# Kernel optimization log

Hardware: AMD Instinct MI355X
Metric: run time of the kernel (lower is better)

The kernel has to match this reference:

```python
import jax, jax.numpy as jnp
import numpy as np


def _conv1x1(x, w, b):
    # x: [B, Cin, T, H, W], w: [Cout, Cin], b: [Cout] -> [B, Cout, T, H, W]
    return jnp.einsum('bcthw,oc->bothw', x, w) + b[None, :, None, None, None]


def setup_inputs() -> dict:
    key = jax.random.key(0)
    ks = jax.random.split(key, 9)
    B, Ci, T, H, W = 2, 128, 4, 32, 32
    Co = 64
    s_in = 1.0 / np.sqrt(Ci)
    s_out = 1.0 / np.sqrt(Co)
    return {
        'z': jax.random.normal(ks[0], (B, Ci, T, H, W), dtype=jnp.float32),
        'w_theta': jax.random.uniform(ks[1], (Co, Ci), jnp.float32, -s_in, s_in),
        'b_theta': jax.random.uniform(ks[2], (Co,), jnp.float32, -s_in, s_in),
        'w_phi': jax.random.uniform(ks[3], (Co, Ci), jnp.float32, -s_in, s_in),
        'b_phi': jax.random.uniform(ks[4], (Co,), jnp.float32, -s_in, s_in),
        'w_psi': jax.random.uniform(ks[5], (Co, Ci), jnp.float32, -s_in, s_in),
        'b_psi': jax.random.uniform(ks[6], (Co,), jnp.float32, -s_in, s_in),
        'w_v': jax.random.uniform(ks[7], (Ci, Co), jnp.float32, -s_out, s_out),
        'b_v': jax.random.uniform(ks[8], (Ci,), jnp.float32, -s_out, s_out),
    }


def reference(z, w_theta, b_theta, w_phi, b_phi, w_psi, b_psi, w_v, b_v):
    B, Ci, T, H, W = z.shape
    Co = w_theta.shape[0]
    N = T * H * W
    # 1x1 conv projections, flattened to [B, Co, N]
    theta = _conv1x1(z, w_theta, b_theta).reshape(B, Co, N)
    phi = _conv1x1(z, w_phi, b_phi).reshape(B, Co, N)
    psi = _conv1x1(z, w_psi, b_psi).reshape(B, Co, N)
    # g = phi^T @ psi : [B, N, N]; normalize with ReLU(g / N)
    g = jnp.einsum('bcn,bcm->bnm', phi, psi)
    norm_g = jax.nn.relu(g / jnp.asarray(N, z.dtype))
    # tmp = norm_g @ theta^T -> [B, N, Co] -> [B, Co, T, H, W]
    tmp = jnp.einsum('bnm,bcm->bcn', norm_g, theta).reshape(B, Co, T, H, W)
    vg = _conv1x1(tmp, w_v, b_v)
    return vg + z
```

## Files before the change

### kernel.cpp

```cpp
#include <hip/hip_runtime.h>


#define NSEQ 4096
#define CI 128
#define CO 64

typedef __attribute__((ext_vector_type(8))) short bf16x8;
typedef __attribute__((ext_vector_type(4))) short bf16x4;
typedef __attribute__((ext_vector_type(4))) float f32x4;
typedef __attribute__((ext_vector_type(16))) float f32x16;

static __device__ inline short f2bf(float f) {
  union { float f; unsigned u; } v; v.f = f;
  unsigned r = v.u + 0x7fffu + ((v.u >> 16) & 1u);
  return (short)(r >> 16);
}
static __device__ inline float bf2f(short s) {
  union { unsigned u; float f; } v; v.u = ((unsigned)(unsigned short)s) << 16;
  return v.f;
}

#define MFMA1632(a, b, c) __builtin_amdgcn_mfma_f32_16x16x32_bf16(a, b, c, 0, 0, 0)
#define MFMA3216(a, b, c) __builtin_amdgcn_mfma_f32_32x32x16_bf16(a, b, c, 0, 0, 0)

#if __has_builtin(__builtin_amdgcn_mfma_f32_16x16x16bf16_1k)
static __device__ inline f32x4 mfma16(bf16x4 a, bf16x4 b, f32x4 c) {
  return __builtin_amdgcn_mfma_f32_16x16x16bf16_1k(a, b, c, 0, 0, 0);
}
#else
static __device__ inline f32x4 mfma16(bf16x4 a, bf16x4 b, f32x4 c) {
  asm("v_mfma_f32_16x16x16_bf16 %0, %1, %2, %0" : "+v"(c) : "v"(a), "v"(b));
  return c;
}
#endif

static __device__ inline unsigned cvt_pk_bf16(float lo, float hi) {
  unsigned d;
  asm("v_cvt_pk_bf16_f32 %0, %1, %2" : "=v"(d) : "v"(lo), "v"(hi));
  return d;
}
static __device__ inline void pl32swap(unsigned& a, unsigned& b) {
  asm("v_permlane32_swap_b32 %0, %1" : "+v"(a), "+v"(b));
}

__global__ __launch_bounds__(256, 2) void proj_kernel(
    const float* __restrict__ z,
    const float* __restrict__ w_th, const float* __restrict__ b_th,
    const float* __restrict__ w_ph, const float* __restrict__ b_ph,
    const float* __restrict__ w_ps, const float* __restrict__ b_ps,
    short* __restrict__ Qg, short* __restrict__ Kg, short* __restrict__ Vt)
{
  const int bid = blockIdx.x;
  const int b = bid >> 8;
  const int n0 = (bid & 255) * 16;
  const int t = threadIdx.x;
  const int w = t >> 6, l = t & 63, lr = l & 15, lg = l >> 4;
  const f32x4 zero4 = {0.f, 0.f, 0.f, 0.f};

  bf16x8 zf[4];
#pragma unroll
  for (int ks = 0; ks < 4; ++ks) {
    const float* zp = z + (size_t)(b * CI + ks * 32 + lg * 8) * NSEQ + n0 + lr;
    float tmp[8];
#pragma unroll
    for (int j = 0; j < 8; ++j) tmp[j] = zp[(size_t)j * NSEQ];
#pragma unroll
    for (int j = 0; j < 8; ++j) zf[ks][j] = f2bf(tmp[j]);
  }

  {
    const float* Wm[2] = {w_ph, w_ps};
    const float* Bm[2] = {b_ph, b_ps};
    short*       Dm[2] = {Qg, Kg};
#pragma unroll
    for (int mt = 0; mt < 2; ++mt) {
      const float sc = (mt == 0) ? (1.0f / 4096.0f) : 1.0f;
      f32x4 acc = zero4;
#pragma unroll
      for (int ks = 0; ks < 4; ++ks) {
        const float* wp = Wm[mt] + (size_t)(w * 16 + lr) * CI + ks * 32 + lg * 8;
        f32x4 x0 = *(const f32x4*)wp;
        f32x4 x1 = *(const f32x4*)(wp + 4);
        bf16x8 wf;
#pragma unroll
        for (int j = 0; j < 4; ++j) { wf[j] = f2bf(x0[j] * sc); wf[4 + j] = f2bf(x1[j] * sc); }
        acc = MFMA1632(wf, zf[ks], acc);
      }
      const f32x4 bias4 = *(const f32x4*)(Bm[mt] + w * 16 + lg * 4);
      bf16x4 pk;
#pragma unroll
      for (int r = 0; r < 4; ++r) pk[r] = f2bf(acc[r] + bias4[r] * sc);
      *(bf16x4*)(Dm[mt] + (size_t)(b * NSEQ + n0 + lr) * CO + w * 16 + lg * 4) = pk;
    }
  }

  {
    f32x4 acc = zero4;
#pragma unroll
    for (int ks = 0; ks < 4; ++ks) {
      const float* wp = w_th + (size_t)(w * 16 + lr) * CI + ks * 32 + lg * 8;
      f32x4 x0 = *(const f32x4*)wp;
      f32x4 x1 = *(const f32x4*)(wp + 4);
      bf16x8 wtf;
#pragma unroll
      for (int j = 0; j < 4; ++j) { wtf[j] = f2bf(x0[j]); wtf[4 + j] = f2bf(x1[j]); }
      acc = MFMA1632(zf[ks], wtf, acc);
    }
    const float bias = b_th[w * 16 + lr];
    bf16x4 pk;
#pragma unroll
    for (int r = 0; r < 4; ++r) pk[r] = f2bf(acc[r] + bias);
    *(bf16x4*)(Vt + (size_t)(b * CO + w * 16 + lr) * NSEQ + n0 + lg * 4) = pk;
  }
}

__global__ __launch_bounds__(256, 3) void attn_kernel(
    const short* __restrict__ Qg, const short* __restrict__ Kg,
    const short* __restrict__ Vt, short* __restrict__ Opart)
{
  __shared__ float red[2][4096];

  const int bid = blockIdx.x;
  const int ms = bid & 7;
  const int rr = bid >> 3;
  const int b  = rr & 1;
  const int nt = rr >> 1;
  const int n0 = nt * 64;
  const int t = threadIdx.x;
  const int w = t >> 6, l = t & 63, lc = l & 31, h = l >> 5;
  const int mw = ms * 512 + w * 128;

  bf16x8 qf[2][4];
  {
    const short* qb = Qg + (size_t)(b * NSEQ + n0 + lc) * CO + h * 8;
#pragma unroll
    for (int nsub = 0; nsub < 2; ++nsub)
#pragma unroll
      for (int ks = 0; ks < 4; ++ks)
        qf[nsub][ks] = *(const bf16x8*)(qb + (size_t)nsub * 32 * CO + ks * 16);
  }

  f32x16 oacc[2][2];
#pragma unroll
  for (int i = 0; i < 2; ++i)
#pragma unroll
    for (int j = 0; j < 2; ++j)
#pragma unroll
      for (int e = 0; e < 16; ++e) oacc[i][j][e] = 0.f;

#pragma unroll
  for (int it = 0; it < 4; ++it) {
    const int m0 = mw + it * 32;

    bf16x8 kf[4];
    {
      const short* kb = Kg + (size_t)(b * NSEQ + m0 + lc) * CO + h * 8;
#pragma unroll
      for (int ks = 0; ks < 4; ++ks) kf[ks] = *(const bf16x8*)(kb + ks * 16);
    }

    f32x16 s0, s1;
#pragma unroll
    for (int e = 0; e < 16; ++e) { s0[e] = 0.f; s1[e] = 0.f; }
#pragma unroll
    for (int ks = 0; ks < 4; ++ks) s0 = MFMA3216(kf[ks], qf[0][ks], s0);
    unsigned pk0[8];
#pragma unroll
    for (int q = 0; q < 8; ++q)
      pk0[q] = cvt_pk_bf16(fmaxf(s0[2 * q], 0.f), fmaxf(s0[2 * q + 1], 0.f));
#pragma unroll
    for (int ks = 0; ks < 4; ++ks) s1 = MFMA3216(kf[ks], qf[1][ks], s1);
    unsigned pk1[8];
#pragma unroll
    for (int q = 0; q < 8; ++q)
      pk1[q] = cvt_pk_bf16(fmaxf(s1[2 * q], 0.f), fmaxf(s1[2 * q + 1], 0.f));

    const short* vb = Vt + (size_t)(b * CO + lc) * NSEQ + m0 + h * 8;
#pragma unroll
    for (int kw = 0; kw < 2; ++kw) {
      unsigned x0 = pk0[4 * kw + 0], y0 = pk0[4 * kw + 2];
      unsigned x1 = pk0[4 * kw + 1], y1 = pk0[4 * kw + 3];
      pl32swap(x0, y0); pl32swap(x1, y1);
      union { unsigned u[4]; bf16x8 v; } pb0 = {{x0, x1, y0, y1}};
      unsigned u0 = pk1[4 * kw + 0], v0 = pk1[4 * kw + 2];
      unsigned u1 = pk1[4 * kw + 1], v1 = pk1[4 * kw + 3];
      pl32swap(u0, v0); pl32swap(u1, v1);
      union { unsigned u[4]; bf16x8 v; } pb1 = {{u0, u1, v0, v1}};

      bf16x8 vf0 = *(const bf16x8*)(vb + kw * 16);
      bf16x8 vf1 = *(const bf16x8*)(vb + (size_t)32 * NSEQ + kw * 16);
      oacc[0][0] = MFMA3216(vf0, pb0.v, oacc[0][0]);
      oacc[1][0] = MFMA3216(vf1, pb0.v, oacc[1][0]);
      oacc[0][1] = MFMA3216(vf0, pb1.v, oacc[0][1]);
      oacc[1][1] = MFMA3216(vf1, pb1.v, oacc[1][1]);
    }
  }

  if (!(w & 1)) {
#pragma unroll
    for (int osub = 0; osub < 2; ++osub)
#pragma unroll
      for (int nsub = 0; nsub < 2; ++nsub)
#pragma unroll
        for (int rb = 0; rb < 4; ++rb) {
          f32x4 v;
#pragma unroll
          for (int r = 0; r < 4; ++r) v[r] = oacc[osub][nsub][rb * 4 + r];
          const int o = osub * 32 + rb * 8 + h * 4;
          const int n = nsub * 32 + lc;
          const int os = o ^ ((n & 15) << 2);
          *(f32x4*)&red[w >> 1][n * 64 + os] = v;
        }
  }
  __syncthreads();
  if (w & 1) {
#pragma unroll
    for (int osub = 0; osub < 2; ++osub)
#pragma unroll
      for (int nsub = 0; nsub < 2; ++nsub)
#pragma unroll
        for (int rb = 0; rb < 4; ++rb) {
          const int o = osub * 32 + rb * 8 + h * 4;
          const int n = nsub * 32 + lc;
          const int os = o ^ ((n & 15) << 2);
          float* p = &red[w >> 1][n * 64 + os];
          f32x4 v = *(f32x4*)p;
#pragma unroll
          for (int r = 0; r < 4; ++r) v[r] += oacc[osub][nsub][rb * 4 + r];
          *(f32x4*)p = v;
        }
  }
  __syncthreads();

  short* gout = Opart + (size_t)((b * 64 + nt) * 8 + ms) * 4096;
#pragma unroll
  for (int pass = 0; pass < 4; ++pass) {
    const int lin = pass * 1024 + t * 4;
    const int n = lin >> 6, os4 = lin & 63;
    f32x4 v0 = *(f32x4*)&red[0][lin];
    f32x4 v1 = *(f32x4*)&red[1][lin];
    const int o = os4 ^ ((n & 15) << 2);
    bf16x4 pkv;
#pragma unroll
    for (int r = 0; r < 4; ++r) pkv[r] = f2bf(v0[r] + v1[r]);
    *(bf16x4*)(gout + n * 64 + o) = pkv;
  }
}

__global__ __launch_bounds__(256, 2) void epi_kernel(
    const short* __restrict__ Opart, const float* __restrict__ w_v,
    const float* __restrict__ b_v, const float* __restrict__ z,
    float* __restrict__ out)
{
  __shared__ float Olds[32 * 65];

  const int bid = blockIdx.x;
  const int b = bid >> 7;
  const int nt32 = bid & 127;
  const int nt = nt32 >> 1, nh2 = nt32 & 1;
  const int t = threadIdx.x;

  {
    const short* src = Opart + (size_t)((b * 64 + nt) * 8) * 4096 + nh2 * 32 * 64;
    const int n = t >> 3, o8 = (t & 7) * 8;
    float acc[8];
#pragma unroll
    for (int j = 0; j < 8; ++j) acc[j] = 0.f;
#pragma unroll
    for (int p = 0; p < 8; ++p) {
      bf16x8 vv = *(const bf16x8*)(src + (size_t)p * 4096 + n * 64 + o8);
#pragma unroll
      for (int j = 0; j < 8; ++j) acc[j] += bf2f(vv[j]);
    }
#pragma unroll
    for (int j = 0; j < 8; ++j) Olds[n * 65 + o8 + j] = acc[j];
  }
  __syncthreads();

  const int w = t >> 6, l = t & 63, lr = l & 15, lg = l >> 4;
  const f32x4 zero4 = {0.f, 0.f, 0.f, 0.f};

  bf16x4 of[2][4];
#pragma unroll
  for (int nh = 0; nh < 2; ++nh)
#pragma unroll
    for (int osub = 0; osub < 4; ++osub)
#pragma unroll
      for (int j = 0; j < 4; ++j)
        of[nh][osub][j] = f2bf(Olds[(nh * 16 + lr) * 65 + osub * 16 + lg * 4 + j]);

#pragma unroll
  for (int c2 = 0; c2 < 2; ++c2) {
    const int cis = w * 2 + c2;
    bf16x4 wfr[4];
#pragma unroll
    for (int osub = 0; osub < 4; ++osub) {
      f32x4 wl = *(const f32x4*)(w_v + (size_t)(cis * 16 + lr) * CO + osub * 16 + lg * 4);
#pragma unroll
      for (int j = 0; j < 4; ++j) wfr[osub][j] = f2bf(wl[j]);
    }
    const f32x4 bv4 = *(const f32x4*)(b_v + cis * 16 + lg * 4);
#pragma unroll
    for (int nh = 0; nh < 2; ++nh) {
      f32x4 e = zero4;
#pragma unroll
      for (int osub = 0; osub < 4; ++osub)
        e = mfma16(wfr[osub], of[nh][osub], e);
#pragma unroll
      for (int r = 0; r < 4; ++r) {
        const int ci = cis * 16 + lg * 4 + r;
        const size_t off = (size_t)(b * CI + ci) * NSEQ + nt32 * 32 + nh * 16 + lr;
        out[off] = e[r] + z[off] + bv4[r];
      }
    }
  }
}

extern "C" void kernel_launch(void* const* d_in, const int* in_sizes, int n_in,
                              void* d_out, int out_size, void* d_ws, size_t ws_size,
                              hipStream_t stream) {
  const float* z    = (const float*)d_in[0];
  const float* w_th = (const float*)d_in[1];
  const float* b_th = (const float*)d_in[2];
  const float* w_ph = (const float*)d_in[3];
  const float* b_ph = (const float*)d_in[4];
  const float* w_ps = (const float*)d_in[5];
  const float* b_ps = (const float*)d_in[6];
  const float* w_v  = (const float*)d_in[7];
  const float* b_v  = (const float*)d_in[8];
  float* out = (float*)d_out;

  short* Qg = (short*)d_ws;
  short* Kg = Qg + 2 * NSEQ * CO;
  short* Vt = Kg + 2 * NSEQ * CO;
  short* Opart = Vt + 2 * NSEQ * CO;

  proj_kernel<<<512, 256, 0, stream>>>(z, w_th, b_th, w_ph, b_ph, w_ps, b_ps,
                                       Qg, Kg, Vt);
  attn_kernel<<<1024, 256, 0, stream>>>(Qg, Kg, Vt, Opart);
  epi_kernel<<<256, 256, 0, stream>>>(Opart, w_v, b_v, z, out);
}
```

Before: 108.9 us.

## Halve attention query tile to 32 rows and double grid for more occupancy

The attention kernel now processes 32 query rows per block instead of 64. That halves the register accumulators and the shared reduction buffer, raises the launch-bounds occupancy hint from 3 to 4, and doubles the grid to 2048 blocks. The epilogue is re-tiled to 16 columns per block with 512 blocks to match the new partial-output layout. The aim is better latency hiding and wave fill across CUs. In exchange, every K and V fragment is now loaded from memory twice as often for the same query work, and there are twice as many partial tiles.

Result: slower. 121.3 us (+11.4%).

```diff
diff --git a/kernel.cpp b/kernel.cpp
--- a/kernel.cpp
+++ b/kernel.cpp
@@ -114,39 +114,34 @@
   }
 }
 
-__global__ __launch_bounds__(256, 3) void attn_kernel(
+__global__ __launch_bounds__(256, 4) void attn_kernel(
     const short* __restrict__ Qg, const short* __restrict__ Kg,
     const short* __restrict__ Vt, short* __restrict__ Opart)
 {
-  __shared__ float red[2][4096];
+  __shared__ float red[2][2048];
 
   const int bid = blockIdx.x;
   const int ms = bid & 7;
-  const int rr = bid >> 3;
-  const int b  = rr & 1;
-  const int nt = rr >> 1;
-  const int n0 = nt * 64;
+  const int u = bid >> 3;
+  const int b = u & 1;
+  const int nt = u >> 1;
+  const int n0 = nt * 32;
   const int t = threadIdx.x;
   const int w = t >> 6, l = t & 63, lc = l & 31, h = l >> 5;
   const int mw = ms * 512 + w * 128;
 
-  bf16x8 qf[2][4];
+  bf16x8 qf[4];
   {
     const short* qb = Qg + (size_t)(b * NSEQ + n0 + lc) * CO + h * 8;
 #pragma unroll
-    for (int nsub = 0; nsub < 2; ++nsub)
-#pragma unroll
-      for (int ks = 0; ks < 4; ++ks)
-        qf[nsub][ks] = *(const bf16x8*)(qb + (size_t)nsub * 32 * CO + ks * 16);
-  }
-
-  f32x16 oacc[2][2];
+    for (int ks = 0; ks < 4; ++ks) qf[ks] = *(const bf16x8*)(qb + ks * 16);
+  }
+
+  f32x16 oacc[2];
 #pragma unroll
   for (int i = 0; i < 2; ++i)
 #pragma unroll
-    for (int j = 0; j < 2; ++j)
-#pragma unroll
-      for (int e = 0; e < 16; ++e) oacc[i][j][e] = 0.f;
+    for (int e = 0; e < 16; ++e) oacc[i][e] = 0.f;
 
 #pragma unroll
   for (int it = 0; it < 4; ++it) {
@@ -159,40 +154,28 @@
       for (int ks = 0; ks < 4; ++ks) kf[ks] = *(const bf16x8*)(kb + ks * 16);
     }
 
-    f32x16 s0, s1;
-#pragma unroll
-    for (int e = 0; e < 16; ++e) { s0[e] = 0.f; s1[e] = 0.f; }
-#pragma unroll
-    for (int ks = 0; ks < 4; ++ks) s0 = MFMA3216(kf[ks], qf[0][ks], s0);
-    unsigned pk0[8];
+    f32x16 s;
+#pragma unroll
+    for (int e = 0; e < 16; ++e) s[e] = 0.f;
+#pragma unroll
+    for (int ks = 0; ks < 4; ++ks) s = MFMA3216(kf[ks], qf[ks], s);
+
+    unsigned pk[8];
 #pragma unroll
     for (int q = 0; q < 8; ++q)
-      pk0[q] = cvt_pk_bf16(fmaxf(s0[2 * q], 0.f), fmaxf(s0[2 * q + 1], 0.f));
-#pragma unroll
-    for (int ks = 0; ks < 4; ++ks) s1 = MFMA3216(kf[ks], qf[1][ks], s1);
-    unsigned pk1[8];
-#pragma unroll
-    for (int q = 0; q < 8; ++q)
-      pk1[q] = cvt_pk_bf16(fmaxf(s1[2 * q], 0.f), fmaxf(s1[2 * q + 1], 0.f));
+      pk[q] = cvt_pk_bf16(fmaxf(s[2 * q], 0.f), fmaxf(s[2 * q + 1], 0.f));
 
     const short* vb = Vt + (size_t)(b * CO + lc) * NSEQ + m0 + h * 8;
 #pragma unroll
     for (int kw = 0; kw < 2; ++kw) {
-      unsigned x0 = pk0[4 * kw + 0], y0 = pk0[4 * kw + 2];
-      unsigned x1 = pk0[4 * kw + 1], y1 = pk0[4 * kw + 3];
+      unsigned x0 = pk[4 * kw + 0], y0 = pk[4 * kw + 2];
+      unsigned x1 = pk[4 * kw + 1], y1 = pk[4 * kw + 3];
       pl32swap(x0, y0); pl32swap(x1, y1);
-      union { unsigned u[4]; bf16x8 v; } pb0 = {{x0, x1, y0, y1}};
-      unsigned u0 = pk1[4 * kw + 0], v0 = pk1[4 * kw + 2];
-      unsigned u1 = pk1[4 * kw + 1], v1 = pk1[4 * kw + 3];
-      pl32swap(u0, v0); pl32swap(u1, v1);
-      union { unsigned u[4]; bf16x8 v; } pb1 = {{u0, u1, v0, v1}};
-
+      union { unsigned u[4]; bf16x8 v; } pb = {{x0, x1, y0, y1}};
       bf16x8 vf0 = *(const bf16x8*)(vb + kw * 16);
       bf16x8 vf1 = *(const bf16x8*)(vb + (size_t)32 * NSEQ + kw * 16);
-      oacc[0][0] = MFMA3216(vf0, pb0.v, oacc[0][0]);
-      oacc[1][0] = MFMA3216(vf1, pb0.v, oacc[1][0]);
-      oacc[0][1] = MFMA3216(vf0, pb1.v, oacc[0][1]);
-      oacc[1][1] = MFMA3216(vf1, pb1.v, oacc[1][1]);
+      oacc[0] = MFMA3216(vf0, pb.v, oacc[0]);
+      oacc[1] = MFMA3216(vf1, pb.v, oacc[1]);
     }
   }
 
@@ -200,41 +183,35 @@
 #pragma unroll
     for (int osub = 0; osub < 2; ++osub)
 #pragma unroll
-      for (int nsub = 0; nsub < 2; ++nsub)
-#pragma unroll
-        for (int rb = 0; rb < 4; ++rb) {
-          f32x4 v;
-#pragma unroll
-          for (int r = 0; r < 4; ++r) v[r] = oacc[osub][nsub][rb * 4 + r];
-          const int o = osub * 32 + rb * 8 + h * 4;
-          const int n = nsub * 32 + lc;
-          const int os = o ^ ((n & 15) << 2);
-          *(f32x4*)&red[w >> 1][n * 64 + os] = v;
-        }
+      for (int rb = 0; rb < 4; ++rb) {
+        f32x4 v;
+#pragma unroll
+        for (int r = 0; r < 4; ++r) v[r] = oacc[osub][rb * 4 + r];
+        const int o = osub * 32 + rb * 8 + h * 4;
+        const int os = o ^ ((lc & 15) << 2);
+        *(f32x4*)&red[w >> 1][lc * 64 + os] = v;
+      }
   }
   __syncthreads();
   if (w & 1) {
 #pragma unroll
     for (int osub = 0; osub < 2; ++osub)
 #pragma unroll
-      for (int nsub = 0; nsub < 2; ++nsub)
-#pragma unroll
-        for (int rb = 0; rb < 4; ++rb) {
-          const int o = osub * 32 + rb * 8 + h * 4;
-          const int n = nsub * 32 + lc;
-          const int os = o ^ ((n & 15) << 2);
-          float* p = &red[w >> 1][n * 64 + os];
-          f32x4 v = *(f32x4*)p;
-#pragma unroll
-          for (int r = 0; r < 4; ++r) v[r] += oacc[osub][nsub][rb * 4 + r];
-          *(f32x4*)p = v;
-        }
+      for (int rb = 0; rb < 4; ++rb) {
+        const int o = osub * 32 + rb * 8 + h * 4;
+        const int os = o ^ ((lc & 15) << 2);
+        float* p = &red[w >> 1][lc * 64 + os];
+        f32x4 v = *(f32x4*)p;
+#pragma unroll
+        for (int r = 0; r < 4; ++r) v[r] += oacc[osub][rb * 4 + r];
+        *(f32x4*)p = v;
+      }
   }
   __syncthreads();
 
-  short* gout = Opart + (size_t)((b * 64 + nt) * 8 + ms) * 4096;
-#pragma unroll
-  for (int pass = 0; pass < 4; ++pass) {
+  short* gout = Opart + (size_t)((b * 128 + nt) * 8 + ms) * 2048;
+#pragma unroll
+  for (int pass = 0; pass < 2; ++pass) {
     const int lin = pass * 1024 + t * 4;
     const int n = lin >> 6, os4 = lin & 63;
     f32x4 v0 = *(f32x4*)&red[0][lin];
@@ -252,42 +229,38 @@
     const float* __restrict__ b_v, const float* __restrict__ z,
     float* __restrict__ out)
 {
-  __shared__ float Olds[32 * 65];
+  __shared__ float Olds[16 * 68];
 
   const int bid = blockIdx.x;
-  const int b = bid >> 7;
-  const int nt32 = bid & 127;
-  const int nt = nt32 >> 1, nh2 = nt32 & 1;
+  const int b = bid >> 8;
+  const int n16 = bid & 255;
+  const int nt = n16 >> 1, sub = n16 & 1;
+  const int n0 = n16 * 16;
   const int t = threadIdx.x;
 
   {
-    const short* src = Opart + (size_t)((b * 64 + nt) * 8) * 4096 + nh2 * 32 * 64;
-    const int n = t >> 3, o8 = (t & 7) * 8;
-    float acc[8];
-#pragma unroll
-    for (int j = 0; j < 8; ++j) acc[j] = 0.f;
+    const short* src = Opart + (size_t)((b * 128 + nt) * 8) * 2048 + sub * 1024;
+    const int n = t >> 4, o4 = (t & 15) * 4;
+    f32x4 acc = {0.f, 0.f, 0.f, 0.f};
 #pragma unroll
     for (int p = 0; p < 8; ++p) {
-      bf16x8 vv = *(const bf16x8*)(src + (size_t)p * 4096 + n * 64 + o8);
-#pragma unroll
-      for (int j = 0; j < 8; ++j) acc[j] += bf2f(vv[j]);
-    }
-#pragma unroll
-    for (int j = 0; j < 8; ++j) Olds[n * 65 + o8 + j] = acc[j];
+      bf16x4 vv = *(const bf16x4*)(src + (size_t)p * 2048 + n * 64 + o4);
+#pragma unroll
+      for (int j = 0; j < 4; ++j) acc[j] += bf2f(vv[j]);
+    }
+    *(f32x4*)&Olds[n * 68 + o4] = acc;
   }
   __syncthreads();
 
   const int w = t >> 6, l = t & 63, lr = l & 15, lg = l >> 4;
   const f32x4 zero4 = {0.f, 0.f, 0.f, 0.f};
 
-  bf16x4 of[2][4];
-#pragma unroll
-  for (int nh = 0; nh < 2; ++nh)
-#pragma unroll
-    for (int osub = 0; osub < 4; ++osub)
-#pragma unroll
-      for (int j = 0; j < 4; ++j)
-        of[nh][osub][j] = f2bf(Olds[(nh * 16 + lr) * 65 + osub * 16 + lg * 4 + j]);
+  bf16x4 of[4];
+#pragma unroll
+  for (int osub = 0; osub < 4; ++osub)
+#pragma unroll
+    for (int j = 0; j < 4; ++j)
+      of[osub][j] = f2bf(Olds[lr * 68 + osub * 16 + lg * 4 + j]);
 
 #pragma unroll
   for (int c2 = 0; c2 < 2; ++c2) {
@@ -300,18 +273,15 @@
       for (int j = 0; j < 4; ++j) wfr[osub][j] = f2bf(wl[j]);
     }
     const f32x4 bv4 = *(const f32x4*)(b_v + cis * 16 + lg * 4);
-#pragma unroll
-    for (int nh = 0; nh < 2; ++nh) {
-      f32x4 e = zero4;
-#pragma unroll
-      for (int osub = 0; osub < 4; ++osub)
-        e = mfma16(wfr[osub], of[nh][osub], e);
-#pragma unroll
-      for (int r = 0; r < 4; ++r) {
-        const int ci = cis * 16 + lg * 4 + r;
-        const size_t off = (size_t)(b * CI + ci) * NSEQ + nt32 * 32 + nh * 16 + lr;
-        out[off] = e[r] + z[off] + bv4[r];
-      }
+    f32x4 e = zero4;
+#pragma unroll
+    for (int osub = 0; osub < 4; ++osub)
+      e = mfma16(wfr[osub], of[osub], e);
+#pragma unroll
+    for (int r = 0; r < 4; ++r) {
+      const int ci = cis * 16 + lg * 4 + r;
+      const size_t off = (size_t)(b * CI + ci) * NSEQ + n0 + lr;
+      out[off] = e[r] + z[off] + bv4[r];
     }
   }
 }
@@ -337,6 +307,6 @@
 
   proj_kernel<<<512, 256, 0, stream>>>(z, w_th, b_th, w_ph, b_ph, w_ps, b_ps,
                                        Qg, Kg, Vt);
-  attn_kernel<<<1024, 256, 0, stream>>>(Qg, Kg, Vt, Opart);
-  epi_kernel<<<256, 256, 0, stream>>>(Opart, w_v, b_v, z, out);
-}
+  attn_kernel<<<2048, 256, 0, stream>>>(Qg, Kg, Vt, Opart);
+  epi_kernel<<<512, 256, 0, stream>>>(Opart, w_v, b_v, z, out);
+}
```
